# Optimization experiments

Measured on AMD Instinct MI355X. Metric: run time of the kernel, lower is better.

The kernel has to match this reference:

```python
import jax, jax.numpy as jnp
import numpy as np

B, C, H, W = 512, 128, 16, 16
WS, HALO, HEADS = 16, 4, 4
HD = C // HEADS            # 32
SCALE = HD ** -0.5
WSH = WS + 2 * HALO        # 24 (padded window size)


def setup_inputs() -> dict:
    key = jax.random.key(0)
    ks = jax.random.split(key, 5)
    return {
        "x": jax.random.normal(ks[0], (B, C, H, W), dtype=jnp.float32),
        "qkv_w": jax.random.normal(ks[1], (3 * C, C), dtype=jnp.float32) * 0.02,
        "qkv_b": jax.random.normal(ks[2], (3 * C,), dtype=jnp.float32) * 0.02,
        "proj_w": jax.random.normal(ks[3], (C, C), dtype=jnp.float32) * 0.02,
        "proj_b": jax.random.normal(ks[4], (C,), dtype=jnp.float32) * 0.02,
    }


def reference(x, qkv_w, qkv_b, proj_w, proj_b):
    b, c, h, w = x.shape
    # reflect pad spatial dims by HALO
    xp = jnp.pad(x, ((0, 0), (0, 0), (HALO, HALO), (HALO, HALO)), mode="reflect")
    hp, wp = h + 2 * HALO, w + 2 * HALO
    # window partition on BHWC with window size WSH (non-overlapping, as in source)
    xw = xp.transpose(0, 2, 3, 1)  # [B, Hp, Wp, C]
    nh, nw = hp // WSH, wp // WSH
    xw = xw.reshape(b, nh, WSH, nw, WSH, c).transpose(0, 1, 3, 2, 4, 5)
    xw = xw.reshape(-1, WSH * WSH, c)  # [nW, 576, C]
    # QKV
    qkv = xw @ qkv_w.T + qkv_b  # [nW, 576, 3C]
    qkv = qkv.reshape(-1, WSH * WSH, 3, HEADS, HD).transpose(2, 0, 3, 1, 4)
    q, k, v = qkv[0], qkv[1], qkv[2]  # [nW, heads, 576, HD]
    # center query slice (contiguous flat slice, faithful to source)
    cs = HALO * WSH + HALO
    csz = WS * WS
    qc = jax.lax.dynamic_slice_in_dim(q, cs, csz, axis=2)  # [nW, heads, 256, HD]
    attn = jax.nn.softmax(jnp.einsum("whqd,whkd->whqk", qc, k) * SCALE, axis=-1)
    out = jnp.einsum("whqk,whkd->wqhd", attn, v).reshape(-1, csz, c)
    out = out @ proj_w.T + proj_b  # [nW, 256, C]
    # window reverse with window size WS over original H, W
    out = out.reshape(b, h // WS, w // WS, WS, WS, c).transpose(0, 1, 3, 2, 4, 5)
    out = out.reshape(b, h, w, c)
    return out.transpose(0, 3, 1, 2)  # [B, C, H, W]
```

## Files before the change

kernel.cpp:

```cpp
#include <hip/hip_runtime.h>
#include <hip/hip_bf16.h>
#include <stdint.h>


typedef short bf16x8 __attribute__((ext_vector_type(8)));
typedef float f32x4 __attribute__((ext_vector_type(4)));

__device__ __forceinline__ unsigned short f2bf(float f) {
  unsigned int u = __builtin_bit_cast(unsigned int, f);
  u += 0x7fffu + ((u >> 16) & 1u);
  return (unsigned short)(u >> 16);
}

__device__ __forceinline__ unsigned int cvt_pk_bf16(float lo, float hi) {
  unsigned int r;
  asm("v_cvt_pk_bf16_f32 %0, %1, %2" : "=v"(r) : "v"(lo), "v"(hi));
  return r;
}

__device__ __forceinline__ f32x4 mfma_16x16x32(bf16x8 a, bf16x8 b, f32x4 c) {
  return __builtin_amdgcn_mfma_f32_16x16x32_bf16(a, b, c, 0, 0, 0);
}

__device__ __forceinline__ void bar_lds() {
  asm volatile("s_waitcnt lgkmcnt(0)\n\ts_barrier" ::: "memory");
}

__device__ __forceinline__ int reflect_s(int tg) {
  int ph = tg / 24;
  int pw = tg - ph * 24;
  int hh = ph - 4; hh = (hh < 0) ? -hh : ((hh > 15) ? 30 - hh : hh);
  int wc = pw - 4; wc = (wc < 0) ? -wc : ((wc > 15) ? 30 - wc : wc);
  return hh * 16 + wc;
}

__global__ void wcvt(const float* __restrict__ qkv_w, const float* __restrict__ proj_w,
                     unsigned short* __restrict__ wq, unsigned short* __restrict__ wp) {
  int i = blockIdx.x * 256 + threadIdx.x;
  if (i < 49152) wq[i] = f2bf(qkv_w[i]);
  if (i < 16384) wp[i] = f2bf(proj_w[i]);
}

__global__ __launch_bounds__(256) void xt_kernel(const float* __restrict__ x,
                                                 unsigned short* __restrict__ xt) {
  __shared__ __align__(16) unsigned int XS[256 * 64];
  const int b = blockIdx.x, tid = threadIdx.x;
  const float* xb = x + (size_t)b * 32768;
  #pragma unroll 4
  for (int it = 0; it < 64; ++it) {
    float f0 = xb[(2 * it) * 256 + tid];
    float f1 = xb[(2 * it + 1) * 256 + tid];
    XS[tid * 64 + (it ^ ((tid & 7) << 2))] =
        (unsigned int)f2bf(f0) | ((unsigned int)f2bf(f1) << 16);
  }
  bar_lds();
  unsigned int* xtd = (unsigned int*)xt + (size_t)b * 16384;
  #pragma unroll
  for (int it = 0; it < 4; ++it) {
    int s = it * 64 + (tid >> 2);
    int cg = (tid & 3) * 4;
    #pragma unroll
    for (int m = 0; m < 4; ++m) {
      uint4 v = *(const uint4*)&XS[s * 64 + (((cg + m) ^ (s & 7)) << 2)];
      *(uint4*)&xtd[s * 64 + (cg + m) * 4] = v;
    }
  }
}

__global__ __launch_bounds__(256) void qkv_kernel(
    const unsigned short* __restrict__ xt, const unsigned short* __restrict__ wq,
    const float* __restrict__ qkv_b, unsigned short* __restrict__ qc,
    unsigned short* __restrict__ kw, unsigned short* __restrict__ vw) {
  __shared__ __align__(16) unsigned short OB[64 * 128];
  const int bid = blockIdx.x;
  const int logical = (bid & 7) * 576 + (bid >> 3);
  const int b = logical / 9;
  const int tile = logical - b * 9;
  const int tid = threadIdx.x;
  const int lane = tid & 63;
  const int wid = tid >> 6;
  const int g = lane >> 4;
  const int r16 = lane & 15;

  const unsigned int* xtd = (const unsigned int*)xt + (size_t)b * 16384;

  int sv[4];
  #pragma unroll
  for (int mt = 0; mt < 4; ++mt)
    sv[mt] = reflect_s(tile * 64 + mt * 16 + r16);

  float bias[6];
  #pragma unroll
  for (int i = 0; i < 6; ++i) bias[i] = qkv_b[(wid + 4 * i) * 16 + r16];

  f32x4 acc[6][4];
  #pragma unroll
  for (int i = 0; i < 6; ++i)
    #pragma unroll
    for (int mt = 0; mt < 4; ++mt) acc[i][mt] = f32x4{0.f, 0.f, 0.f, 0.f};

  #pragma unroll
  for (int kt = 0; kt < 4; ++kt) {
    bf16x8 afr[4];
    #pragma unroll
    for (int mt = 0; mt < 4; ++mt)
      afr[mt] = __builtin_bit_cast(bf16x8, *(const uint4*)&xtd[sv[mt] * 64 + kt * 16 + g * 4]);
    #pragma unroll
    for (int i = 0; i < 6; ++i) {
      int n = (wid + 4 * i) * 16 + r16;
      bf16x8 bfr = __builtin_bit_cast(bf16x8, *(const uint4*)(wq + n * 128 + kt * 32 + g * 8));
      #pragma unroll
      for (int mt = 0; mt < 4; ++mt)
        acc[i][mt] = mfma_16x16x32(afr[mt], bfr, acc[i][mt]);
    }
  }

  #pragma unroll
  for (int sel = 0; sel < 3; ++sel) {
    bar_lds();
    #pragma unroll
    for (int j = 0; j < 2; ++j) {
      const int i = sel * 2 + j;
      int dcol = (wid + 4 * j) * 16 + r16;
      #pragma unroll
      for (int mt = 0; mt < 4; ++mt)
        #pragma unroll
        for (int rr = 0; rr < 4; ++rr)
          OB[(mt * 16 + 4 * g + rr) * 128 + dcol] = f2bf(acc[i][mt][rr] + bias[i]);
    }
    bar_lds();
    #pragma unroll
    for (int it = 0; it < 4; ++it) {
      int flat = it * 2048 + tid * 8;
      int tokl = flat >> 7, d0 = flat & 127;
      int tg = tile * 64 + tokl;
      uint4 val = *(const uint4*)&OB[tokl * 128 + d0];
      if (sel == 0) {
        int qi = tg - 100;
        if ((unsigned)qi < 256u)
          *(uint4*)(qc + ((size_t)b * 256 + qi) * 128 + d0) = val;
      } else if (sel == 1) {
        *(uint4*)(kw + ((size_t)b * 576 + tg) * 128 + d0) = val;
      } else {
        *(uint4*)(vw + ((size_t)b * 576 + tg) * 128 + d0) = val;
      }
    }
  }
}

__global__ __launch_bounds__(256) void attn_kernel(
    const unsigned short* __restrict__ qc, const unsigned short* __restrict__ kw,
    const unsigned short* __restrict__ vw, unsigned short* __restrict__ ao) {
  __shared__ __align__(16) unsigned int KF[4 * 192 * 4];
  __shared__ __align__(16) unsigned short VT[32 * 200];
  const int bh = blockIdx.x;
  const int tid = threadIdx.x;
  const int lane = tid & 63;
  const int wid = tid >> 6;
  const int g = lane >> 4;
  const int r16 = lane & 15;
  const int qb = wid * 64;
  const int b = bh >> 2, h = bh & 3;

  const unsigned short* qcb = qc + (size_t)b * 256 * 128 + h * 32;
  const unsigned short* kb = kw + (size_t)b * 576 * 128 + h * 32;
  const unsigned short* vb = vw + (size_t)b * 576 * 128 + h * 32;

  unsigned int kreg[12], vreg[12];
  {
    const unsigned int* ks = (const unsigned int*)kb;
    const unsigned int* vs = (const unsigned int*)vb;
    #pragma unroll
    for (int it = 0; it < 12; ++it) {
      int f = it * 256 + tid;
      int kv = f >> 4, cu = f & 15;
      kreg[it] = ks[kv * 64 + cu];
      vreg[it] = vs[kv * 64 + cu];
    }
  }

  bf16x8 qf[4];
  #pragma unroll
  for (int qnt = 0; qnt < 4; ++qnt)
    qf[qnt] = __builtin_bit_cast(bf16x8, *(const uint4*)(qcb + (size_t)(qb + qnt * 16 + r16) * 128 + g * 8));

  float ls[4];
  #pragma unroll
  for (int i = 0; i < 4; ++i) ls[i] = 0.f;
  f32x4 oa[2][4];
  #pragma unroll
  for (int i = 0; i < 2; ++i)
    #pragma unroll
    for (int j = 0; j < 4; ++j) oa[i][j] = f32x4{0.f, 0.f, 0.f, 0.f};

  const float KE = 0.17677669529663687f * 1.4426950408889634f;

  for (int ch = 0; ch < 3; ++ch) {
    if (ch) bar_lds();
    #pragma unroll
    for (int it = 0; it < 12; ++it) {
      int f = it * 256 + tid;
      int kv = f >> 4, cu = f & 15;
      KF[(cu >> 2) * 768 + kv * 4 + (cu & 3)] = kreg[it];
      int kv32 = kv & 31;
      int idx = (kv >> 5) * 32 + ((kv32 & 15) >> 2) * 8 + (kv32 >> 4) * 4 + (kv32 & 3);
      unsigned int pk = vreg[it];
      VT[(2 * cu) * 200 + idx] = (unsigned short)(pk & 0xffffu);
      VT[(2 * cu + 1) * 200 + idx] = (unsigned short)(pk >> 16);
    }
    bar_lds();
    if (ch < 2) {
      const unsigned int* ks = (const unsigned int*)(kb + (size_t)(ch + 1) * 192 * 128);
      const unsigned int* vs = (const unsigned int*)(vb + (size_t)(ch + 1) * 192 * 128);
      #pragma unroll
      for (int it = 0; it < 12; ++it) {
        int f = it * 256 + tid;
        int kv = f >> 4, cu = f & 15;
        kreg[it] = ks[kv * 64 + cu];
        vreg[it] = vs[kv * 64 + cu];
      }
    }

    for (int kvt2 = 0; kvt2 < 6; ++kvt2) {
      bf16x8 kf0 = __builtin_bit_cast(bf16x8, *(const uint4*)&KF[g * 768 + (kvt2 * 32 + r16) * 4]);
      bf16x8 kf1 = __builtin_bit_cast(bf16x8, *(const uint4*)&KF[g * 768 + (kvt2 * 32 + 16 + r16) * 4]);
      f32x4 zero = f32x4{0.f, 0.f, 0.f, 0.f};
      f32x4 st0[4], st1[4];
      #pragma unroll
      for (int qnt = 0; qnt < 4; ++qnt) {
        st0[qnt] = mfma_16x16x32(kf0, qf[qnt], zero);
        st1[qnt] = mfma_16x16x32(kf1, qf[qnt], zero);
      }

      bf16x8 pf[4];
      #pragma unroll
      for (int qnt = 0; qnt < 4; ++qnt) {
        f32x4 s0 = st0[qnt], s1 = st1[qnt];
        float p[8];
        #pragma unroll
        for (int j = 0; j < 4; ++j) p[j] = __builtin_amdgcn_exp2f(s0[j] * KE);
        #pragma unroll
        for (int j = 0; j < 4; ++j) p[4 + j] = __builtin_amdgcn_exp2f(s1[j] * KE);
        float ts = ((p[0] + p[1]) + (p[2] + p[3])) + ((p[4] + p[5]) + (p[6] + p[7]));
        ls[qnt] += ts;
        uint4 pk4;
        pk4.x = cvt_pk_bf16(p[0], p[1]);
        pk4.y = cvt_pk_bf16(p[2], p[3]);
        pk4.z = cvt_pk_bf16(p[4], p[5]);
        pk4.w = cvt_pk_bf16(p[6], p[7]);
        pf[qnt] = __builtin_bit_cast(bf16x8, pk4);
      }
      #pragma unroll
      for (int dmt = 0; dmt < 2; ++dmt) {
        int d = dmt * 16 + r16;
        bf16x8 vf = __builtin_bit_cast(bf16x8, *(const uint4*)&VT[d * 200 + kvt2 * 32 + g * 8]);
        #pragma unroll
        for (int qnt = 0; qnt < 4; ++qnt)
          oa[dmt][qnt] = mfma_16x16x32(vf, pf[qnt], oa[dmt][qnt]);
      }
    }
  }

  #pragma unroll
  for (int qnt = 0; qnt < 4; ++qnt) {
    float l = ls[qnt];
    l += __shfl_xor(l, 16);
    l += __shfl_xor(l, 32);
    float rl = 1.0f / l;
    int q = qb + qnt * 16 + r16;
    #pragma unroll
    for (int dmt = 0; dmt < 2; ++dmt) {
      #pragma unroll
      for (int rr = 0; rr < 4; ++rr) {
        int d = dmt * 16 + 4 * g + rr;
        ao[((size_t)b * 256 + q) * 128 + h * 32 + d] = f2bf(oa[dmt][qnt][rr] * rl);
      }
    }
  }
}

__global__ __launch_bounds__(256) void proj_kernel(
    const unsigned short* __restrict__ ao, const unsigned short* __restrict__ wp,
    const float* __restrict__ proj_b, float* __restrict__ out) {
  __shared__ __align__(16) unsigned int A32[64 * 64];
  const int wg = blockIdx.x;
  const int b = wg >> 2;
  const int mq = wg & 3;
  const int tid = threadIdx.x;
  const int lane = tid & 63;
  const int wid = tid >> 6;
  const int g = lane >> 4;
  const int r16 = lane & 15;

  const unsigned int* asrc = (const unsigned int*)(ao + ((size_t)b * 256 + mq * 64) * 128);
  #pragma unroll
  for (int it = 0; it < 4; ++it) {
    int f = it * 256 + tid;
    int row = f >> 4, q4 = f & 15;
    uint4 v = *(const uint4*)&asrc[row * 64 + q4 * 4];
    *(uint4*)&A32[row * 64 + ((q4 * 4) ^ ((row & 7) << 2))] = v;
  }
  bar_lds();

  f32x4 acc[2][4];
  #pragma unroll
  for (int nt = 0; nt < 2; ++nt)
    #pragma unroll
    for (int mt = 0; mt < 4; ++mt) acc[nt][mt] = f32x4{0.f, 0.f, 0.f, 0.f};

  for (int kt = 0; kt < 4; ++kt) {
    bf16x8 afr[4];
    #pragma unroll
    for (int mt = 0; mt < 4; ++mt) {
      int row = mt * 16 + r16;
      int cub = (kt * 16 + g * 4) ^ ((row & 7) << 2);
      afr[mt] = __builtin_bit_cast(bf16x8, *(const uint4*)&A32[row * 64 + cub]);
    }
    #pragma unroll
    for (int nt = 0; nt < 2; ++nt) {
      int n = wid * 32 + nt * 16 + r16;
      bf16x8 bfr = __builtin_bit_cast(bf16x8, *(const uint4*)(wp + n * 128 + kt * 32 + g * 8));
      #pragma unroll
      for (int mt = 0; mt < 4; ++mt)
        acc[nt][mt] = mfma_16x16x32(afr[mt], bfr, acc[nt][mt]);
    }
  }

  #pragma unroll
  for (int nt = 0; nt < 2; ++nt) {
    int c = wid * 32 + nt * 16 + r16;
    float bv = proj_b[c];
    #pragma unroll
    for (int mt = 0; mt < 4; ++mt) {
      int t0 = mq * 64 + mt * 16 + 4 * g;
      float4 o;
      o.x = acc[nt][mt][0] + bv;
      o.y = acc[nt][mt][1] + bv;
      o.z = acc[nt][mt][2] + bv;
      o.w = acc[nt][mt][3] + bv;
      *(float4*)&out[((size_t)b * 128 + c) * 256 + t0] = o;
    }
  }
}

extern "C" void kernel_launch(void* const* d_in, const int* in_sizes, int n_in,
                              void* d_out, int out_size, void* d_ws, size_t ws_size,
                              hipStream_t stream) {
  const float* x = (const float*)d_in[0];
  const float* qkv_w = (const float*)d_in[1];
  const float* qkv_b = (const float*)d_in[2];
  const float* proj_w = (const float*)d_in[3];
  const float* proj_b = (const float*)d_in[4];
  float* out = (float*)d_out;

  unsigned short* ws16 = (unsigned short*)d_ws;
  unsigned short* wp = ws16;
  unsigned short* wq = ws16 + 16384;
  unsigned short* xtp = ws16 + 65536;
  unsigned short* qcp = xtp + (size_t)16777216;
  unsigned short* kp = qcp + (size_t)16777216;
  unsigned short* vp = kp + (size_t)37748736;
  unsigned short* ap = xtp;

  hipLaunchKernelGGL(wcvt, dim3(192), dim3(256), 0, stream, qkv_w, proj_w, wq, wp);
  hipLaunchKernelGGL(xt_kernel, dim3(512), dim3(256), 0, stream, x, xtp);
  hipLaunchKernelGGL(qkv_kernel, dim3(4608), dim3(256), 0, stream, xtp, wq, qkv_b, qcp, kp, vp);
  hipLaunchKernelGGL(attn_kernel, dim3(2048), dim3(256), 0, stream, qcp, kp, vp, ap);
  hipLaunchKernelGGL(proj_kernel, dim3(2048), dim3(256), 0, stream, ap, wp, proj_b, out);
}
```

Before: 260.4 us.

## Fuse QKV projection into per-head attention kernel, dropping K/V global round-trip

Merges the QKV GEMM kernel and the attention kernel into one kernel per (batch, head). Each block computes its head's Q slice and, chunk by chunk, its K/V slices straight from the transposed input into LDS, then runs the attention on that chunk. The goal is to stop writing K/V/Q to global memory and reading them back, which removes large HBM traffic and one launch. The cost is more LDS per block, which may lower occupancy, and less latency hiding since the GEMM and attention phases are separated by barriers. The ordering also puts each next chunk's GEMM after the current attention phase in the same wave.

Result: slower. 376.4 us (+44.5%).

```diff
diff --git a/kernel.cpp b/kernel.cpp
--- a/kernel.cpp
+++ b/kernel.cpp
@@ -67,160 +67,126 @@
   }
 }
 
-__global__ __launch_bounds__(256) void qkv_kernel(
+__global__ __launch_bounds__(256) void fused_kernel(
     const unsigned short* __restrict__ xt, const unsigned short* __restrict__ wq,
-    const float* __restrict__ qkv_b, unsigned short* __restrict__ qc,
-    unsigned short* __restrict__ kw, unsigned short* __restrict__ vw) {
-  __shared__ __align__(16) unsigned short OB[64 * 128];
+    const float* __restrict__ qkv_b, unsigned short* __restrict__ ao) {
+  __shared__ __align__(16) unsigned short POOL[38144];
+  unsigned short* QC = POOL;
+  unsigned short* OBK = POOL + 10240;
+  unsigned short* OBV = POOL + 17920;
+  unsigned int* KF = (unsigned int*)(POOL + 25600);
+  unsigned short* VT = POOL + 31744;
+
   const int bid = blockIdx.x;
-  const int logical = (bid & 7) * 576 + (bid >> 3);
-  const int b = logical / 9;
-  const int tile = logical - b * 9;
-  const int tid = threadIdx.x;
-  const int lane = tid & 63;
-  const int wid = tid >> 6;
-  const int g = lane >> 4;
-  const int r16 = lane & 15;
-
-  const unsigned int* xtd = (const unsigned int*)xt + (size_t)b * 16384;
-
-  int sv[4];
-  #pragma unroll
-  for (int mt = 0; mt < 4; ++mt)
-    sv[mt] = reflect_s(tile * 64 + mt * 16 + r16);
-
-  float bias[6];
-  #pragma unroll
-  for (int i = 0; i < 6; ++i) bias[i] = qkv_b[(wid + 4 * i) * 16 + r16];
-
-  f32x4 acc[6][4];
-  #pragma unroll
-  for (int i = 0; i < 6; ++i)
-    #pragma unroll
-    for (int mt = 0; mt < 4; ++mt) acc[i][mt] = f32x4{0.f, 0.f, 0.f, 0.f};
-
-  #pragma unroll
-  for (int kt = 0; kt < 4; ++kt) {
-    bf16x8 afr[4];
-    #pragma unroll
-    for (int mt = 0; mt < 4; ++mt)
-      afr[mt] = __builtin_bit_cast(bf16x8, *(const uint4*)&xtd[sv[mt] * 64 + kt * 16 + g * 4]);
-    #pragma unroll
-    for (int i = 0; i < 6; ++i) {
-      int n = (wid + 4 * i) * 16 + r16;
-      bf16x8 bfr = __builtin_bit_cast(bf16x8, *(const uint4*)(wq + n * 128 + kt * 32 + g * 8));
-      #pragma unroll
-      for (int mt = 0; mt < 4; ++mt)
-        acc[i][mt] = mfma_16x16x32(afr[mt], bfr, acc[i][mt]);
-    }
-  }
-
-  #pragma unroll
-  for (int sel = 0; sel < 3; ++sel) {
-    bar_lds();
-    #pragma unroll
-    for (int j = 0; j < 2; ++j) {
-      const int i = sel * 2 + j;
-      int dcol = (wid + 4 * j) * 16 + r16;
-      #pragma unroll
-      for (int mt = 0; mt < 4; ++mt)
-        #pragma unroll
-        for (int rr = 0; rr < 4; ++rr)
-          OB[(mt * 16 + 4 * g + rr) * 128 + dcol] = f2bf(acc[i][mt][rr] + bias[i]);
-    }
-    bar_lds();
-    #pragma unroll
-    for (int it = 0; it < 4; ++it) {
-      int flat = it * 2048 + tid * 8;
-      int tokl = flat >> 7, d0 = flat & 127;
-      int tg = tile * 64 + tokl;
-      uint4 val = *(const uint4*)&OB[tokl * 128 + d0];
-      if (sel == 0) {
-        int qi = tg - 100;
-        if ((unsigned)qi < 256u)
-          *(uint4*)(qc + ((size_t)b * 256 + qi) * 128 + d0) = val;
-      } else if (sel == 1) {
-        *(uint4*)(kw + ((size_t)b * 576 + tg) * 128 + d0) = val;
-      } else {
-        *(uint4*)(vw + ((size_t)b * 576 + tg) * 128 + d0) = val;
-      }
-    }
-  }
-}
-
-__global__ __launch_bounds__(256) void attn_kernel(
-    const unsigned short* __restrict__ qc, const unsigned short* __restrict__ kw,
-    const unsigned short* __restrict__ vw, unsigned short* __restrict__ ao) {
-  __shared__ __align__(16) unsigned int KF[4 * 192 * 4];
-  __shared__ __align__(16) unsigned short VT[32 * 200];
-  const int bh = blockIdx.x;
+  const int slot = bid >> 3;
+  const int b = (bid & 7) * 64 + (slot & 63);
+  const int h = slot >> 6;
   const int tid = threadIdx.x;
   const int lane = tid & 63;
   const int wid = tid >> 6;
   const int g = lane >> 4;
   const int r16 = lane & 15;
   const int qb = wid * 64;
-  const int b = bh >> 2, h = bh & 3;
-
-  const unsigned short* qcb = qc + (size_t)b * 256 * 128 + h * 32;
-  const unsigned short* kb = kw + (size_t)b * 576 * 128 + h * 32;
-  const unsigned short* vb = vw + (size_t)b * 576 * 128 + h * 32;
-
-  unsigned int kreg[12], vreg[12];
+
+  const unsigned int* xtd = (const unsigned int*)xt + (size_t)b * 16384;
+  const float KE = 0.17677669529663687f * 1.4426950408889634f;
+
   {
-    const unsigned int* ks = (const unsigned int*)kb;
-    const unsigned int* vs = (const unsigned int*)vb;
+    f32x4 qacc[4][2];
+    #pragma unroll
+    for (int mt = 0; mt < 4; ++mt)
+      #pragma unroll
+      for (int nt = 0; nt < 2; ++nt) qacc[mt][nt] = f32x4{0.f, 0.f, 0.f, 0.f};
+    #pragma unroll
+    for (int kt = 0; kt < 4; ++kt) {
+      bf16x8 Bf[2];
+      #pragma unroll
+      for (int nt = 0; nt < 2; ++nt)
+        Bf[nt] = __builtin_bit_cast(
+            bf16x8, *(const uint4*)(wq + (h * 32 + nt * 16 + r16) * 128 + kt * 32 + g * 8));
+      #pragma unroll
+      for (int mt = 0; mt < 4; ++mt) {
+        int sv = reflect_s(100 + qb + mt * 16 + r16);
+        bf16x8 A = __builtin_bit_cast(bf16x8, *(const uint4*)&xtd[sv * 64 + kt * 16 + g * 4]);
+        #pragma unroll
+        for (int nt = 0; nt < 2; ++nt) qacc[mt][nt] = mfma_16x16x32(A, Bf[nt], qacc[mt][nt]);
+      }
+    }
+    #pragma unroll
+    for (int nt = 0; nt < 2; ++nt) {
+      float bv = qkv_b[h * 32 + nt * 16 + r16];
+      #pragma unroll
+      for (int mt = 0; mt < 4; ++mt)
+        #pragma unroll
+        for (int rr = 0; rr < 4; ++rr)
+          QC[(qb + mt * 16 + 4 * g + rr) * 40 + nt * 16 + r16] = f2bf(qacc[mt][nt][rr] + bv);
+    }
+  }
+  __syncthreads();
+  bf16x8 qf[4];
+  #pragma unroll
+  for (int qnt = 0; qnt < 4; ++qnt)
+    qf[qnt] = __builtin_bit_cast(bf16x8, *(const uint4*)&QC[(qb + qnt * 16 + r16) * 40 + g * 8]);
+
+  float ls[4] = {0.f, 0.f, 0.f, 0.f};
+  f32x4 oa[2][4];
+  #pragma unroll
+  for (int i = 0; i < 2; ++i)
+    #pragma unroll
+    for (int j = 0; j < 4; ++j) oa[i][j] = f32x4{0.f, 0.f, 0.f, 0.f};
+
+  auto GPH = [&](int c) {
+    f32x4 acc[3][4];
+    #pragma unroll
+    for (int m = 0; m < 3; ++m)
+      #pragma unroll
+      for (int j = 0; j < 4; ++j) acc[m][j] = f32x4{0.f, 0.f, 0.f, 0.f};
+    #pragma unroll
+    for (int kt = 0; kt < 4; ++kt) {
+      bf16x8 Bf[4];
+      #pragma unroll
+      for (int j = 0; j < 4; ++j) {
+        int n_abs = (1 + (j >> 1)) * 128 + h * 32 + (j & 1) * 16 + r16;
+        Bf[j] = __builtin_bit_cast(bf16x8, *(const uint4*)(wq + n_abs * 128 + kt * 32 + g * 8));
+      }
+      #pragma unroll
+      for (int m = 0; m < 3; ++m) {
+        int sv = reflect_s(c * 192 + (wid * 3 + m) * 16 + r16);
+        bf16x8 A = __builtin_bit_cast(bf16x8, *(const uint4*)&xtd[sv * 64 + kt * 16 + g * 4]);
+        #pragma unroll
+        for (int j = 0; j < 4; ++j) acc[m][j] = mfma_16x16x32(A, Bf[j], acc[m][j]);
+      }
+    }
+    #pragma unroll
+    for (int j = 0; j < 4; ++j) {
+      float bv = qkv_b[(1 + (j >> 1)) * 128 + h * 32 + (j & 1) * 16 + r16];
+      int dcol = (j & 1) * 16 + r16;
+      unsigned short* dst = (j < 2) ? OBK : OBV;
+      #pragma unroll
+      for (int m = 0; m < 3; ++m)
+        #pragma unroll
+        for (int rr = 0; rr < 4; ++rr) {
+          int tokL = (wid * 3 + m) * 16 + 4 * g + rr;
+          dst[tokL * 40 + dcol] = f2bf(acc[m][j][rr] + bv);
+        }
+    }
+  };
+
+  auto RST = [&]() {
     #pragma unroll
     for (int it = 0; it < 12; ++it) {
       int f = it * 256 + tid;
       int kv = f >> 4, cu = f & 15;
-      kreg[it] = ks[kv * 64 + cu];
-      vreg[it] = vs[kv * 64 + cu];
-    }
-  }
-
-  bf16x8 qf[4];
-  #pragma unroll
-  for (int qnt = 0; qnt < 4; ++qnt)
-    qf[qnt] = __builtin_bit_cast(bf16x8, *(const uint4*)(qcb + (size_t)(qb + qnt * 16 + r16) * 128 + g * 8));
-
-  float ls[4];
-  #pragma unroll
-  for (int i = 0; i < 4; ++i) ls[i] = 0.f;
-  f32x4 oa[2][4];
-  #pragma unroll
-  for (int i = 0; i < 2; ++i)
-    #pragma unroll
-    for (int j = 0; j < 4; ++j) oa[i][j] = f32x4{0.f, 0.f, 0.f, 0.f};
-
-  const float KE = 0.17677669529663687f * 1.4426950408889634f;
-
-  for (int ch = 0; ch < 3; ++ch) {
-    if (ch) bar_lds();
-    #pragma unroll
-    for (int it = 0; it < 12; ++it) {
-      int f = it * 256 + tid;
-      int kv = f >> 4, cu = f & 15;
-      KF[(cu >> 2) * 768 + kv * 4 + (cu & 3)] = kreg[it];
+      KF[(cu >> 2) * 768 + kv * 4 + (cu & 3)] = *(const unsigned int*)&OBK[kv * 40 + 2 * cu];
       int kv32 = kv & 31;
       int idx = (kv >> 5) * 32 + ((kv32 & 15) >> 2) * 8 + (kv32 >> 4) * 4 + (kv32 & 3);
-      unsigned int pk = vreg[it];
+      unsigned int pk = *(const unsigned int*)&OBV[kv * 40 + 2 * cu];
       VT[(2 * cu) * 200 + idx] = (unsigned short)(pk & 0xffffu);
       VT[(2 * cu + 1) * 200 + idx] = (unsigned short)(pk >> 16);
     }
-    bar_lds();
-    if (ch < 2) {
-      const unsigned int* ks = (const unsigned int*)(kb + (size_t)(ch + 1) * 192 * 128);
-      const unsigned int* vs = (const unsigned int*)(vb + (size_t)(ch + 1) * 192 * 128);
-      #pragma unroll
-      for (int it = 0; it < 12; ++it) {
-        int f = it * 256 + tid;
-        int kv = f >> 4, cu = f & 15;
-        kreg[it] = ks[kv * 64 + cu];
-        vreg[it] = vs[kv * 64 + cu];
-      }
-    }
-
+  };
+
+  auto APH = [&]() {
     for (int kvt2 = 0; kvt2 < 6; ++kvt2) {
       bf16x8 kf0 = __builtin_bit_cast(bf16x8, *(const uint4*)&KF[g * 768 + (kvt2 * 32 + r16) * 4]);
       bf16x8 kf1 = __builtin_bit_cast(bf16x8, *(const uint4*)&KF[g * 768 + (kvt2 * 32 + 16 + r16) * 4]);
@@ -231,7 +197,6 @@
         st0[qnt] = mfma_16x16x32(kf0, qf[qnt], zero);
         st1[qnt] = mfma_16x16x32(kf1, qf[qnt], zero);
       }
-
       bf16x8 pf[4];
       #pragma unroll
       for (int qnt = 0; qnt < 4; ++qnt) {
@@ -241,8 +206,7 @@
         for (int j = 0; j < 4; ++j) p[j] = __builtin_amdgcn_exp2f(s0[j] * KE);
         #pragma unroll
         for (int j = 0; j < 4; ++j) p[4 + j] = __builtin_amdgcn_exp2f(s1[j] * KE);
-        float ts = ((p[0] + p[1]) + (p[2] + p[3])) + ((p[4] + p[5]) + (p[6] + p[7]));
-        ls[qnt] += ts;
+        ls[qnt] += ((p[0] + p[1]) + (p[2] + p[3])) + ((p[4] + p[5]) + (p[6] + p[7]));
         uint4 pk4;
         pk4.x = cvt_pk_bf16(p[0], p[1]);
         pk4.y = cvt_pk_bf16(p[2], p[3]);
@@ -259,7 +223,21 @@
           oa[dmt][qnt] = mfma_16x16x32(vf, pf[qnt], oa[dmt][qnt]);
       }
     }
-  }
+  };
+
+  GPH(0);
+  __syncthreads();
+  RST();
+  __syncthreads();
+  APH(); GPH(1);
+  __syncthreads();
+  RST();
+  __syncthreads();
+  APH(); GPH(2);
+  __syncthreads();
+  RST();
+  __syncthreads();
+  APH();
 
   #pragma unroll
   for (int qnt = 0; qnt < 4; ++qnt) {
@@ -357,14 +335,10 @@
   unsigned short* wp = ws16;
   unsigned short* wq = ws16 + 16384;
   unsigned short* xtp = ws16 + 65536;
-  unsigned short* qcp = xtp + (size_t)16777216;
-  unsigned short* kp = qcp + (size_t)16777216;
-  unsigned short* vp = kp + (size_t)37748736;
-  unsigned short* ap = xtp;
+  unsigned short* ap = xtp + (size_t)16777216;
 
   hipLaunchKernelGGL(wcvt, dim3(192), dim3(256), 0, stream, qkv_w, proj_w, wq, wp);
   hipLaunchKernelGGL(xt_kernel, dim3(512), dim3(256), 0, stream, x, xtp);
-  hipLaunchKernelGGL(qkv_kernel, dim3(4608), dim3(256), 0, stream, xtp, wq, qkv_b, qcp, kp, vp);
-  hipLaunchKernelGGL(attn_kernel, dim3(2048), dim3(256), 0, stream, qcp, kp, vp, ap);
+  hipLaunchKernelGGL(fused_kernel, dim3(2048), dim3(256), 0, stream, xtp, wq, qkv_b, ap);
   hipLaunchKernelGGL(proj_kernel, dim3(2048), dim3(256), 0, stream, ap, wp, proj_b, out);
 }
```
